# Kernel tuning notes

Hardware: AMD Instinct MI355X
Metric: run time of the kernel (lower is better)

## Reference

```python
import jax, jax.numpy as jnp
import numpy as np

N_NODES = 100000
N_EDGES = 3200000
N_GRAPHS = 1024


def _glorot(key, shape):
    fan_in, fan_out = shape[0], shape[1]
    lim = (6.0 / (fan_in + fan_out)) ** 0.5
    return jax.random.uniform(key, shape, jnp.float32, -lim, lim)


def setup_inputs() -> dict:
    key = jax.random.key(0)
    ks = jax.random.split(key, 12)
    x = jax.random.normal(ks[0], (N_NODES, 2), jnp.float32)
    edge_attr = jax.random.normal(ks[1], (N_EDGES, 1), jnp.float32)
    edge_index = jax.random.randint(ks[2], (2, N_EDGES), 0, N_NODES, jnp.int64)
    batch = jnp.sort(jax.random.randint(ks[3], (N_NODES,), 0, N_GRAPHS, jnp.int64))
    params = {
        'w_node': _glorot(ks[4], (2, 32)),   'b_node': jnp.zeros((32,), jnp.float32),
        'w_edge': _glorot(ks[5], (1, 32)),   'b_edge': jnp.zeros((32,), jnp.float32),
        'w1': _glorot(ks[6], (32, 64)),      'b1': jnp.zeros((64,), jnp.float32),
        'w2': _glorot(ks[7], (64, 64)),      'b2': jnp.zeros((64,), jnp.float32),
        'wf1': _glorot(ks[8], (64, 32)),     'bf1': jnp.zeros((32,), jnp.float32),
        'wf2': _glorot(ks[9], (32, 1)),      'bf2': jnp.zeros((1,), jnp.float32),
    }
    return {'x': x, 'edge_attr': edge_attr, 'edge_index': edge_index, 'batch': batch, **params}


def gcn_conv(x, edge_index, w, b):
    # PyG GCNConv: out = D^{-1/2} (A + I) D^{-1/2} (x @ w) + b
    n = x.shape[0]
    xw = x @ w  # [N, F_out]
    loops = jnp.arange(n, dtype=edge_index.dtype)
    src = jnp.concatenate([edge_index[0], loops])  # messages flow src -> dst
    dst = jnp.concatenate([edge_index[1], loops])
    deg = jax.ops.segment_sum(jnp.ones_like(dst, dtype=xw.dtype), dst, num_segments=n)
    dis = jnp.where(deg > 0, jax.lax.rsqrt(jnp.maximum(deg, 1e-12)), 0.0)
    norm = dis[src] * dis[dst]  # [E+N]
    msgs = xw[src] * norm[:, None]  # gather + scale, [E+N, F_out]
    out = jax.ops.segment_sum(msgs, dst, num_segments=n)
    return out + b


def reference(x, edge_attr, edge_index, batch,
              w_node, b_node, w_edge, b_edge,
              w1, b1, w2, b2, wf1, bf1, wf2, bf2):
    h = jax.nn.relu(x @ w_node + b_node)               # [N, 32]
    e = jax.nn.relu(edge_attr @ w_edge + b_edge)       # [E, 32] (computed, unused downstream as in source)
    h = jax.nn.relu(gcn_conv(h, edge_index, w1, b1))   # [N, 64]
    h = jax.nn.relu(gcn_conv(h, edge_index, w2, b2))   # [N, 64]
    # global mean pool over graphs
    sums = jax.ops.segment_sum(h, batch, num_segments=N_GRAPHS)  # [G, 64]
    cnts = jax.ops.segment_sum(jnp.ones((h.shape[0],), h.dtype), batch, num_segments=N_GRAPHS)
    pooled = sums / jnp.maximum(cnts, 1.0)[:, None]
    g = jax.nn.relu(pooled @ wf1 + bf1)                # [G, 32]
    out = g @ wf2 + bf2                                # [G, 1]
    return out
```

## Files before the change

kernel.cpp:

```cpp
#include <hip/hip_runtime.h>
#include <hip/hip_fp16.h>


typedef float vfloat4 __attribute__((ext_vector_type(4)));

#define NBMAX 512
#define BCAP 12288
#define CAPL 10240

__global__ void k_initcur(int* __restrict__ bcur) {
    bcur[threadIdx.x] = threadIdx.x * BCAP;
}

__global__ void k_passA(const int* __restrict__ ei, int* __restrict__ bcur,
                        unsigned int* __restrict__ pairBuf, int E) {
    __shared__ int h[NBMAX];
    __shared__ int base[NBMAX];
    const int T = 256, EPT = 32;
    int chunk = blockIdx.x * (T * EPT);
    int t = threadIdx.x;
    h[t] = 0; h[t + 256] = 0;
    __syncthreads();
    int nE = min(E - chunk, T * EPT);
    for (int i = t; i < nE; i += T)
        atomicAdd(&h[ei[E + chunk + i] >> 8], 1);
    __syncthreads();
    for (int bb = t; bb < NBMAX; bb += T) {
        int c = h[bb];
        base[bb] = c > 0 ? atomicAdd(&bcur[bb], c) : 0;
        h[bb] = 0;
    }
    __syncthreads();
    for (int i = t; i < nE; i += T) {
        int s = ei[chunk + i];
        int d = ei[E + chunk + i];
        int bb = d >> 8;
        int pos = base[bb] + atomicAdd(&h[bb], 1);
        pairBuf[pos] = ((unsigned int)(d & 255) << 24) | (unsigned int)s;
    }
}

__global__ void k_passB(const int* __restrict__ bcur,
                        const unsigned int* __restrict__ pairBuf,
                        int* __restrict__ rowPtr, float* __restrict__ dis,
                        int* __restrict__ srcIdx, const float* __restrict__ x,
                        float4* __restrict__ p, int N, int E) {
    __shared__ unsigned int eLds[CAPL];
    __shared__ int hist[256];
    __shared__ int scan[256];
    int b = blockIdx.x;
    int t = threadIdx.x;
    int count = bcur[b] - b * BCAP;
    const unsigned int* src = pairBuf + (size_t)b * BCAP;
    int part = 0;
    for (int i = t; i < b; i += 256) part += bcur[i] - i * BCAP;
    scan[t] = part;
    __syncthreads();
    for (int o = 128; o > 0; o >>= 1) {
        if (t < o) scan[t] += scan[t + o];
        __syncthreads();
    }
    int gbase = scan[0];
    __syncthreads();
    hist[t] = 0;
    int nStage = min(count, CAPL);
    for (int i = t; i < nStage; i += 256) eLds[i] = __builtin_nontemporal_load(src + i);
    __syncthreads();
    for (int i = t; i < nStage; i += 256) atomicAdd(&hist[eLds[i] >> 24], 1);
    for (int i = CAPL + t; i < count; i += 256)
        atomicAdd(&hist[__builtin_nontemporal_load(src + i) >> 24], 1);
    __syncthreads();
    int c = hist[t];
    scan[t] = c;
    __syncthreads();
    for (int o = 1; o < 256; o <<= 1) {
        int v = (t >= o) ? scan[t - o] : 0;
        __syncthreads();
        scan[t] += v;
        __syncthreads();
    }
    int excl = scan[t] - c;
    int node = (b << 8) + t;
    float dval = rsqrtf((float)c + 1.0f);
    if (node < N) {
        rowPtr[node] = gbase + excl;
        dis[node] = dval;
        float4 pv;
        pv.x = x[2 * node]; pv.y = x[2 * node + 1]; pv.z = dval; pv.w = 0.f;
        p[node] = pv;
        if (node == N - 1) rowPtr[N] = E;
    }
    hist[t] = excl;
    __syncthreads();
    for (int i = t; i < nStage; i += 256) {
        unsigned int e = eLds[i];
        int pos = atomicAdd(&hist[e >> 24], 1);
        srcIdx[gbase + pos] = (int)(e & 0xFFFFFFu);
    }
    for (int i = CAPL + t; i < count; i += 256) {
        unsigned int e = __builtin_nontemporal_load(src + i);
        int pos = atomicAdd(&hist[e >> 24], 1);
        srcIdx[gbase + pos] = (int)(e & 0xFFFFFFu);
    }
}

__global__ void k_agg32x(const int* __restrict__ rowPtr, const int* __restrict__ srcIdx,
                         const float4* __restrict__ p, const float* __restrict__ wn,
                         const float* __restrict__ bn, const float* __restrict__ w1,
                         const float* __restrict__ b1, __half* __restrict__ hOut, int N) {
    constexpr int RPI = 8, U = 4, CH = RPI * U;
    int wid = (blockIdx.x * blockDim.x + threadIdx.x) >> 6;
    if (wid >= N) return;
    int lane = threadIdx.x & 63;
    int q = lane & 7;
    int r = lane >> 3;
    float wn0[4], wn1[4], bnv[4];
#pragma unroll
    for (int j = 0; j < 4; ++j) {
        wn0[j] = wn[4 * q + j];
        wn1[j] = wn[32 + 4 * q + j];
        bnv[j] = bn[4 * q + j];
    }
    float4 pd = p[wid];
    float accv[4] = {0.f, 0.f, 0.f, 0.f};
    if (r == 0) {
#pragma unroll
        for (int j = 0; j < 4; ++j) {
            float v = fmaf(pd.x, wn0[j], fmaf(pd.y, wn1[j], bnv[j]));
            accv[j] = fmaxf(v, 0.f) * pd.z;
        }
    }
    int beg = rowPtr[wid], end = rowPtr[wid + 1];
    if (end > beg) {
        int last = end - 1;
        for (int base = beg; base < end; base += CH) {
            int s[U];
            float m[U];
#pragma unroll
            for (int u = 0; u < U; ++u) {
                int i = base + r + u * RPI;
                m[u] = (i < end) ? 1.f : 0.f;
                s[u] = __builtin_nontemporal_load(srcIdx + min(i, last));
            }
            float4 ps[U];
#pragma unroll
            for (int u = 0; u < U; ++u) ps[u] = p[s[u]];
#pragma unroll
            for (int u = 0; u < U; ++u) {
                float scale = ps[u].z * m[u];
#pragma unroll
                for (int j = 0; j < 4; ++j) {
                    float v = fmaf(ps[u].x, wn0[j], fmaf(ps[u].y, wn1[j], bnv[j]));
                    accv[j] = fmaf(fmaxf(v, 0.f), scale, accv[j]);
                }
            }
        }
    }
#pragma unroll
    for (int mk = 8; mk < 64; mk <<= 1) {
#pragma unroll
        for (int j = 0; j < 4; ++j) accv[j] += __shfl_xor(accv[j], mk);
    }
    int f = lane;
    float s = 0.f;
#pragma unroll
    for (int q2 = 0; q2 < 8; ++q2) {
#pragma unroll
        for (int j = 0; j < 4; ++j) {
            float bv = __shfl(accv[j], q2);
            s = fmaf(bv, w1[(4 * q2 + j) * 64 + f], s);
        }
    }
    float dv = pd.z;
    float h = fmaxf(fmaf(dv, s, b1[f]), 0.f) * dv;
    hOut[(size_t)wid * 64 + f] = __float2half(h);
}

__global__ void k_agg64h(const int* __restrict__ rowPtr, const int* __restrict__ srcIdx,
                         const __half* __restrict__ y, const float* __restrict__ dis,
                         float* __restrict__ z, int N) {
    constexpr int RPI = 8, U = 4, CH = RPI * U;
    int wid = (blockIdx.x * blockDim.x + threadIdx.x) >> 6;
    if (wid >= N) return;
    int lane = threadIdx.x & 63;
    int q = lane & 7;
    int r = lane >> 3;
    const float4* yq = (const float4*)y;
    float acc[8] = {0.f, 0.f, 0.f, 0.f, 0.f, 0.f, 0.f, 0.f};
    if (r == 0) {
        float4 a = yq[(size_t)wid * 8 + q];
        union { float4 f4; __half2 h2[4]; } cv; cv.f4 = a;
#pragma unroll
        for (int j = 0; j < 4; ++j) {
            float2 f = __half22float2(cv.h2[j]);
            acc[2 * j] = f.x; acc[2 * j + 1] = f.y;
        }
    }
    int beg = rowPtr[wid], end = rowPtr[wid + 1];
    if (end > beg) {
        int last = end - 1;
        for (int base = beg; base < end; base += CH) {
            int s[U];
            float m[U];
#pragma unroll
            for (int u = 0; u < U; ++u) {
                int i = base + r + u * RPI;
                m[u] = (i < end) ? 1.f : 0.f;
                s[u] = __builtin_nontemporal_load(srcIdx + min(i, last));
            }
#pragma unroll
            for (int u = 0; u < U; ++u) {
                float4 a = yq[(size_t)s[u] * 8 + q];
                union { float4 f4; __half2 h2[4]; } cv; cv.f4 = a;
#pragma unroll
                for (int j = 0; j < 4; ++j) {
                    float2 f = __half22float2(cv.h2[j]);
                    acc[2 * j]     = fmaf(f.x, m[u], acc[2 * j]);
                    acc[2 * j + 1] = fmaf(f.y, m[u], acc[2 * j + 1]);
                }
            }
        }
    }
#pragma unroll
    for (int mk = 8; mk < 64; mk <<= 1) {
#pragma unroll
        for (int j = 0; j < 8; ++j) acc[j] += __shfl_xor(acc[j], mk);
    }
    if (r == 0) {
        float dv = dis[wid];
        float4 o0 = {acc[0] * dv, acc[1] * dv, acc[2] * dv, acc[3] * dv};
        float4 o1 = {acc[4] * dv, acc[5] * dv, acc[6] * dv, acc[7] * dv};
        float4* zp = (float4*)(z + (size_t)wid * 64 + q * 8);
        zp[0] = o0;
        zp[1] = o1;
    }
}

__global__ void k_poolhead(const float* __restrict__ z2, const float* __restrict__ w2,
                           const float* __restrict__ b2, const int* __restrict__ batch,
                           const float* __restrict__ wf1, const float* __restrict__ bf1,
                           const float* __restrict__ wf2, const float* __restrict__ bf2,
                           float* __restrict__ out, int N) {
    __shared__ float red[4][64];
    __shared__ float pooled[64];
    __shared__ float gv[32];
    __shared__ int range[2];
    int g = blockIdx.x;
    int t = threadIdx.x;
    if (t < 2) {
        int target = g + t;
        int lo = 0, hi = N;
        while (lo < hi) {
            int mid = (lo + hi) >> 1;
            if (batch[mid] < target) lo = mid + 1; else hi = mid;
        }
        range[t] = lo;
    }
    __syncthreads();
    int s = range[0], e = range[1];
    int w = t >> 6, f = t & 63;
    float wcol[64];
#pragma unroll
    for (int k = 0; k < 64; ++k) wcol[k] = w2[k * 64 + f];
    float bf = b2[f];
    float acc = 0.f;
    for (int n = s + w; n < e; n += 4) {
        const float4* zr = (const float4*)(z2 + (size_t)n * 64);
        float h = bf;
#pragma unroll
        for (int kq = 0; kq < 16; ++kq) {
            float4 zv = zr[kq];
            h += zv.x * wcol[4 * kq + 0];
            h += zv.y * wcol[4 * kq + 1];
            h += zv.z * wcol[4 * kq + 2];
            h += zv.w * wcol[4 * kq + 3];
        }
        acc += fmaxf(h, 0.f);
    }
    red[w][f] = acc;
    __syncthreads();
    if (t < 64) {
        float c = (float)(e - s);
        c = c > 1.f ? c : 1.f;
        pooled[t] = (red[0][t] + red[1][t] + red[2][t] + red[3][t]) / c;
    }
    __syncthreads();
    if (t < 32) {
        float sv = bf1[t];
#pragma unroll
        for (int k = 0; k < 64; ++k) sv += pooled[k] * wf1[k * 32 + t];
        gv[t] = fmaxf(sv, 0.f);
    }
    __syncthreads();
    if (t == 0) {
        float sv = bf2[0];
#pragma unroll
        for (int j = 0; j < 32; ++j) sv += gv[j] * wf2[j];
        out[g] = sv;
    }
}

extern "C" void kernel_launch(void* const* d_in, const int* in_sizes, int n_in,
                              void* d_out, int out_size, void* d_ws, size_t ws_size,
                              hipStream_t stream) {
    const float* x      = (const float*)d_in[0];
    const int*   ei     = (const int*)d_in[2];
    const int*   batch  = (const int*)d_in[3];
    const float* w_node = (const float*)d_in[4];
    const float* b_node = (const float*)d_in[5];
    const float* w1  = (const float*)d_in[8];
    const float* b1  = (const float*)d_in[9];
    const float* w2  = (const float*)d_in[10];
    const float* b2  = (const float*)d_in[11];
    const float* wf1 = (const float*)d_in[12];
    const float* bf1 = (const float*)d_in[13];
    const float* wf2 = (const float*)d_in[14];
    const float* bf2 = (const float*)d_in[15];
    float* out = (float*)d_out;

    const int N = in_sizes[0] / 2;
    const int E = in_sizes[2] / 2;
    const int G = out_size;
    const int NB = (N + 255) >> 8;

    auto align256 = [](size_t v) { return (v + 255) & ~(size_t)255; };
    char* ws = (char*)d_ws;
    size_t off = 0;
    float*  dis     = (float*)(ws + off);  off += align256((size_t)N * 4);
    int*    rowPtr  = (int*)(ws + off);    off += align256((size_t)(N + 1) * 4);
    int*    bcur    = (int*)(ws + off);    off += align256((size_t)NBMAX * 4);
    int*    srcIdx  = (int*)(ws + off);    off += align256((size_t)E * 4);
    float*  region1 = (float*)(ws + off);  off += align256((size_t)N * 64 * 4);
    __half* hT1     = (__half*)(ws + off); off += align256((size_t)N * 64 * 2);
    float4* p       = (float4*)(ws + off); off += align256((size_t)N * 16);

    unsigned int* pairBuf = (unsigned int*)region1;
    float* z2 = region1;

    const int B = 256;

    k_initcur<<<1, NBMAX, 0, stream>>>(bcur);
    {
        int nblk = (E + B * 32 - 1) / (B * 32);
        k_passA<<<nblk, B, 0, stream>>>(ei, bcur, pairBuf, E);
    }
    k_passB<<<NB, B, 0, stream>>>(bcur, pairBuf, rowPtr, dis, srcIdx, x, p, N, E);

    k_agg32x<<<(N * 64 + B - 1) / B, B, 0, stream>>>(rowPtr, srcIdx, p, w_node, b_node,
                                                     w1, b1, hT1, N);

    k_agg64h<<<(N * 64 + B - 1) / B, B, 0, stream>>>(rowPtr, srcIdx, hT1, dis, z2, N);

    k_poolhead<<<G, B, 0, stream>>>(z2, w2, b2, batch, wf1, bf1, wf2, bf2, out, N);
}
```

Measured before the change: 260.8 us.

## Precompute scaled fp16 node embeddings in passB and gather them in first aggregation

```diff
diff --git a/kernel.cpp b/kernel.cpp
--- a/kernel.cpp
+++ b/kernel.cpp
@@ -1,8 +1,6 @@
 #include <hip/hip_runtime.h>
 #include <hip/hip_fp16.h>
 
-
-typedef float vfloat4 __attribute__((ext_vector_type(4)));
 
 #define NBMAX 512
 #define BCAP 12288
@@ -44,7 +42,8 @@
                         const unsigned int* __restrict__ pairBuf,
                         int* __restrict__ rowPtr, float* __restrict__ dis,
                         int* __restrict__ srcIdx, const float* __restrict__ x,
-                        float4* __restrict__ p, int N, int E) {
+                        const float* __restrict__ wn, const float* __restrict__ bn,
+                        __half* __restrict__ h0, int N, int E) {
     __shared__ unsigned int eLds[CAPL];
     __shared__ int hist[256];
     __shared__ int scan[256];
@@ -85,9 +84,6 @@
     if (node < N) {
         rowPtr[node] = gbase + excl;
         dis[node] = dval;
-        float4 pv;
-        pv.x = x[2 * node]; pv.y = x[2 * node + 1]; pv.z = dval; pv.w = 0.f;
-        p[node] = pv;
         if (node == N - 1) rowPtr[N] = E;
     }
     hist[t] = excl;
@@ -102,32 +98,43 @@
         int pos = atomicAdd(&hist[e >> 24], 1);
         srcIdx[gbase + pos] = (int)(e & 0xFFFFFFu);
     }
-}
-
-__global__ void k_agg32x(const int* __restrict__ rowPtr, const int* __restrict__ srcIdx,
-                         const float4* __restrict__ p, const float* __restrict__ wn,
-                         const float* __restrict__ bn, const float* __restrict__ w1,
-                         const float* __restrict__ b1, __half* __restrict__ hOut, int N) {
-    constexpr int RPI = 8, U = 4, CH = RPI * U;
+    if (node < N) {
+        float x0 = x[2 * node], x1 = x[2 * node + 1];
+        __half2 hv[16];
+#pragma unroll
+        for (int j = 0; j < 32; j += 2) {
+            float v0 = fmaf(x0, wn[j],     fmaf(x1, wn[32 + j],     bn[j]));
+            float v1 = fmaf(x0, wn[j + 1], fmaf(x1, wn[32 + j + 1], bn[j + 1]));
+            v0 = fmaxf(v0, 0.f) * dval;
+            v1 = fmaxf(v1, 0.f) * dval;
+            hv[j >> 1] = __floats2half2_rn(v0, v1);
+        }
+        float4* dst = (float4*)(h0 + (size_t)node * 32);
+        const float4* sv = (const float4*)hv;
+#pragma unroll
+        for (int k = 0; k < 4; ++k) dst[k] = sv[k];
+    }
+}
+
+__global__ void k_agg32f(const int* __restrict__ rowPtr, const int* __restrict__ srcIdx,
+                         const __half* __restrict__ y, const float* __restrict__ dis,
+                         const float* __restrict__ w1, const float* __restrict__ b1,
+                         __half* __restrict__ hOut, int N) {
+    constexpr int RPI = 16, U = 2, CH = RPI * U;
     int wid = (blockIdx.x * blockDim.x + threadIdx.x) >> 6;
     if (wid >= N) return;
     int lane = threadIdx.x & 63;
-    int q = lane & 7;
-    int r = lane >> 3;
-    float wn0[4], wn1[4], bnv[4];
-#pragma unroll
-    for (int j = 0; j < 4; ++j) {
-        wn0[j] = wn[4 * q + j];
-        wn1[j] = wn[32 + 4 * q + j];
-        bnv[j] = bn[4 * q + j];
-    }
-    float4 pd = p[wid];
-    float accv[4] = {0.f, 0.f, 0.f, 0.f};
+    int q = lane & 3;
+    int r = lane >> 2;
+    const float4* yq = (const float4*)y;
+    float acc[8] = {0.f, 0.f, 0.f, 0.f, 0.f, 0.f, 0.f, 0.f};
     if (r == 0) {
+        float4 a = yq[(size_t)wid * 4 + q];
+        union { float4 f4; __half2 h2[4]; } cv; cv.f4 = a;
 #pragma unroll
         for (int j = 0; j < 4; ++j) {
-            float v = fmaf(pd.x, wn0[j], fmaf(pd.y, wn1[j], bnv[j]));
-            accv[j] = fmaxf(v, 0.f) * pd.z;
+            float2 f = __half22float2(cv.h2[j]);
+            acc[2 * j] = f.x; acc[2 * j + 1] = f.y;
         }
     }
     int beg = rowPtr[wid], end = rowPtr[wid + 1];
@@ -142,36 +149,35 @@
                 m[u] = (i < end) ? 1.f : 0.f;
                 s[u] = __builtin_nontemporal_load(srcIdx + min(i, last));
             }
-            float4 ps[U];
-#pragma unroll
-            for (int u = 0; u < U; ++u) ps[u] = p[s[u]];
 #pragma unroll
             for (int u = 0; u < U; ++u) {
-                float scale = ps[u].z * m[u];
+                float4 a = yq[(size_t)s[u] * 4 + q];
+                union { float4 f4; __half2 h2[4]; } cv; cv.f4 = a;
 #pragma unroll
                 for (int j = 0; j < 4; ++j) {
-                    float v = fmaf(ps[u].x, wn0[j], fmaf(ps[u].y, wn1[j], bnv[j]));
-                    accv[j] = fmaf(fmaxf(v, 0.f), scale, accv[j]);
+                    float2 f = __half22float2(cv.h2[j]);
+                    acc[2 * j]     = fmaf(f.x, m[u], acc[2 * j]);
+                    acc[2 * j + 1] = fmaf(f.y, m[u], acc[2 * j + 1]);
                 }
             }
         }
     }
 #pragma unroll
-    for (int mk = 8; mk < 64; mk <<= 1) {
-#pragma unroll
-        for (int j = 0; j < 4; ++j) accv[j] += __shfl_xor(accv[j], mk);
+    for (int mk = 4; mk < 64; mk <<= 1) {
+#pragma unroll
+        for (int j = 0; j < 8; ++j) acc[j] += __shfl_xor(acc[j], mk);
     }
     int f = lane;
     float s = 0.f;
 #pragma unroll
-    for (int q2 = 0; q2 < 8; ++q2) {
-#pragma unroll
-        for (int j = 0; j < 4; ++j) {
-            float bv = __shfl(accv[j], q2);
-            s = fmaf(bv, w1[(4 * q2 + j) * 64 + f], s);
-        }
-    }
-    float dv = pd.z;
+    for (int q2 = 0; q2 < 4; ++q2) {
+#pragma unroll
+        for (int j = 0; j < 8; ++j) {
+            float bv = __shfl(acc[j], q2);
+            s = fmaf(bv, w1[(8 * q2 + j) * 64 + f], s);
+        }
+    }
+    float dv = dis[wid];
     float h = fmaxf(fmaf(dv, s, b1[f]), 0.f) * dv;
     hOut[(size_t)wid * 64 + f] = __float2half(h);
 }
@@ -332,7 +338,7 @@
     int*    srcIdx  = (int*)(ws + off);    off += align256((size_t)E * 4);
     float*  region1 = (float*)(ws + off);  off += align256((size_t)N * 64 * 4);
     __half* hT1     = (__half*)(ws + off); off += align256((size_t)N * 64 * 2);
-    float4* p       = (float4*)(ws + off); off += align256((size_t)N * 16);
+    __half* h0h     = (__half*)(ws + off); off += align256((size_t)N * 32 * 2);
 
     unsigned int* pairBuf = (unsigned int*)region1;
     float* z2 = region1;
@@ -344,9 +350,10 @@
         int nblk = (E + B * 32 - 1) / (B * 32);
         k_passA<<<nblk, B, 0, stream>>>(ei, bcur, pairBuf, E);
     }
-    k_passB<<<NB, B, 0, stream>>>(bcur, pairBuf, rowPtr, dis, srcIdx, x, p, N, E);
-
-    k_agg32x<<<(N * 64 + B - 1) / B, B, 0, stream>>>(rowPtr, srcIdx, p, w_node, b_node,
+    k_passB<<<NB, B, 0, stream>>>(bcur, pairBuf, rowPtr, dis, srcIdx,
+                                  x, w_node, b_node, h0h, N, E);
+
+    k_agg32f<<<(N * 64 + B - 1) / B, B, 0, stream>>>(rowPtr, srcIdx, h0h, dis,
                                                      w1, b1, hT1, N);
 
     k_agg64h<<<(N * 64 + B - 1) / B, B, 0, stream>>>(rowPtr, srcIdx, hT1, dis, z2, N);
```

After: 264.1 us. About the same (+1.3%).
